# Kernel optimization log

Hardware: AMD Instinct MI355X
Metric: run time of the kernel (lower is better)

The kernel has to match this reference:

```python
import jax, jax.numpy as jnp
import numpy as np

N = 50000      # nodes
D = 128        # in_dim
O = 128        # out_dim
MAX_DEG = 32   # degrees uniform in [0, MAX_DEG]


def setup_inputs() -> dict:
    rng = np.random.default_rng(0)
    deg = rng.integers(0, MAX_DEG + 1, size=N)          # includes deg==0 nodes
    dst = np.repeat(np.arange(N), deg)                  # target node per edge (grouped, like the buckets)
    E = dst.shape[0]                                    # ~800000
    src = rng.integers(0, N, size=E)                    # neighbor index per edge (flat neighbor_list)

    key = jax.random.key(0)
    k1, k2, k3, k4 = jax.random.split(key, 4)
    scale = jnp.float32(1.0 / np.sqrt(D))
    return {
        "x":  jax.random.normal(k1, (N, D), jnp.float32),
        "Wg": jax.random.normal(k2, (O, D), jnp.float32) * scale,  # global_lin.weight
        "Wl": jax.random.normal(k3, (O, D), jnp.float32) * scale,  # local_lin.weight
        "Ws": jax.random.normal(k4, (O, D), jnp.float32) * scale,  # self_lin.weight
        "b":  jnp.zeros((O,), jnp.float32),                        # bias param
        "src": jnp.asarray(src, jnp.int32),
        "dst": jnp.asarray(dst, jnp.int32),
        "deg": jnp.asarray(deg, jnp.int32),
    }


def reference(x, Wg, Wl, Ws, b, src, dst, deg):
    n = x.shape[0]
    # global branch: applied to every node
    g_out = x @ Wg.T                                           # [N, O]
    # mean-aggregate neighbor features (gather + segment-sum == the per-bucket view().mean())
    neigh_sum = jax.ops.segment_sum(x[src], dst, num_segments=n)   # [N, D]
    degf = jnp.maximum(deg, 1).astype(x.dtype)[:, None]
    neigh_mean = neigh_sum * (1.0 / degf)                       # [N, D]
    # local + self branches only for deg > 0 (deg==0 bucket keeps just global_out)
    mask = (deg > 0).astype(x.dtype)[:, None]                   # [N, 1]
    out = g_out + mask * (neigh_mean @ Wl.T + x @ Ws.T) + b
    # dropout is identity in eval mode; ELU activation
    return jax.nn.elu(out)
```

## Files before the change

kernel.cpp:

```cpp
#include <hip/hip_runtime.h>
#include <cstdint>
#include <cstddef>

#define KCAT  384
#define AST   392
#define NPB   16
#define PREPV 128

typedef __attribute__((ext_vector_type(8))) short bf16x8;
typedef __attribute__((ext_vector_type(4))) float f32x4;

static __device__ __forceinline__ unsigned short f2bf(float f) {
    unsigned int u = __builtin_bit_cast(unsigned int, f);
    unsigned int lsb = (u >> 16) & 1u;
    u += 0x7fffu + lsb;
    return (unsigned short)(u >> 16);
}
static __device__ __forceinline__ float bfhi(unsigned int u) {
    return __builtin_bit_cast(float, u & 0xFFFF0000u);
}
static __device__ __forceinline__ float bflo(unsigned int u) {
    return __builtin_bit_cast(float, u << 16);
}
static __device__ __forceinline__ void acc8(float* a, const uint4& v) {
    a[0] += bflo(v.x); a[1] += bfhi(v.x); a[2] += bflo(v.y); a[3] += bfhi(v.y);
    a[4] += bflo(v.z); a[5] += bfhi(v.z); a[6] += bflo(v.w); a[7] += bfhi(v.w);
}

__global__ __launch_bounds__(256)
void prep(const float* __restrict__ x, const float* __restrict__ Wg,
          const float* __restrict__ Wl, const float* __restrict__ Ws,
          const int* __restrict__ dst, unsigned short* __restrict__ V,
          unsigned short* __restrict__ xb, int* __restrict__ blkoff,
          int total8, int nblk, int noffb, int E) {
    const int bx = blockIdx.x;
    const int t  = threadIdx.x;
    if (bx < PREPV) {
        const int o = bx;
        float v = (t < 128) ? Wg[o * 128 + t] : Wl[o * 128 + (t - 128)];
        V[o * KCAT + t] = f2bf(v);
        if (t < 128) V[o * KCAT + 256 + t] = f2bf(Ws[o * 128 + t]);
    } else if (bx < PREPV + noffb) {
        int b = (bx - PREPV) * 256 + t;
        if (b < nblk) {
            int target = b * NPB;
            int lo = 0, hi = E;
            while (lo < hi) { int mid = (lo + hi) >> 1; if (dst[mid] < target) lo = mid + 1; else hi = mid; }
            blkoff[b] = lo;
        }
    } else {
        int gid = (bx - PREPV - noffb) * 256 + t;
        if (gid < total8) {
            const float4* px = (const float4*)x + (size_t)gid * 2;
            float4 a = px[0], bq = px[1];
            uint4 u;
            u.x = (unsigned)f2bf(a.x)  | ((unsigned)f2bf(a.y)  << 16);
            u.y = (unsigned)f2bf(a.z)  | ((unsigned)f2bf(a.w)  << 16);
            u.z = (unsigned)f2bf(bq.x) | ((unsigned)f2bf(bq.y) << 16);
            u.w = (unsigned)f2bf(bq.z) | ((unsigned)f2bf(bq.w) << 16);
            ((uint4*)xb)[gid] = u;
        }
    }
}

__global__ __launch_bounds__(256, 8)
void fused_agg_gemm(const unsigned short* __restrict__ xb, const int* __restrict__ src,
                    const int* __restrict__ deg, const int* __restrict__ blkoff,
                    const unsigned short* __restrict__ V, const float* __restrict__ bias,
                    float* __restrict__ out, int N) {
    __shared__ __align__(16) unsigned short Ash[NPB * AST];
    __shared__ int sstart[NPB];
    __shared__ int sdeg[NPB];
    const int t    = threadIdx.x;
    const int wv   = t >> 6;
    const int lane = t & 63;
    const int c    = lane & 15;
    const int p    = lane >> 4;
    const int base = blockIdx.x * NPB;

    if (wv == 0) {
        int lo = blkoff[blockIdx.x];
        int n  = base + lane;
        int dg = (lane < NPB && n < N) ? deg[n] : 0;
        int incl = dg;
#pragma unroll
        for (int off = 1; off < NPB; off <<= 1) {
            int v = __shfl_up(incl, off, 64);
            if (lane >= off) incl += v;
        }
        if (lane < NPB) { sstart[lane] = lo + incl - dg; sdeg[lane] = dg; }
    }
    __syncthreads();

    const uint4* x4 = (const uint4*)xb;
    int dgs[4], sss[4], idxs[4];
#pragma unroll
    for (int r = 0; r < 4; ++r) {
        int row = wv * 4 + r;
        dgs[r] = sdeg[row];
        sss[r] = sstart[row];
        idxs[r] = 0;
        if (lane < dgs[r]) idxs[r] = src[sss[r] + lane];
    }
#pragma unroll
    for (int r = 0; r < 4; ++r) {
        const int row = wv * 4 + r;
        const int n   = base + row;
        const int d   = dgs[r];
        uint4 xv = {0, 0, 0, 0};
        if (p == 1 && n < N) xv = x4[(size_t)n * 16 + c];

        float a[8] = {0,0,0,0,0,0,0,0};
        float b[8] = {0,0,0,0,0,0,0,0};
        {
            int r0 = __shfl(idxs[r], p, 64);
            int r1 = __shfl(idxs[r], p + 4, 64);
            int r2 = __shfl(idxs[r], p + 8, 64);
            int r3 = __shfl(idxs[r], p + 12, 64);
            uint4 v0 = x4[(size_t)r0 * 16 + c];
            uint4 v1 = x4[(size_t)r1 * 16 + c];
            uint4 v2 = x4[(size_t)r2 * 16 + c];
            uint4 v3 = x4[(size_t)r3 * 16 + c];
            if (p < d)      acc8(a, v0);
            if (p + 4 < d)  acc8(b, v1);
            if (p + 8 < d)  acc8(a, v2);
            if (p + 12 < d) acc8(b, v3);
        }
        if (d > 16) {
            int e0 = 16 + p;
            int r0 = __shfl(idxs[r], e0, 64);
            int r1 = __shfl(idxs[r], e0 + 4, 64);
            int r2 = __shfl(idxs[r], e0 + 8, 64);
            int r3 = __shfl(idxs[r], e0 + 12, 64);
            uint4 v0 = x4[(size_t)r0 * 16 + c];
            uint4 v1 = x4[(size_t)r1 * 16 + c];
            uint4 v2 = x4[(size_t)r2 * 16 + c];
            uint4 v3 = x4[(size_t)r3 * 16 + c];
            if (e0 < d)      acc8(a, v0);
            if (e0 + 4 < d)  acc8(b, v1);
            if (e0 + 8 < d)  acc8(a, v2);
            if (e0 + 12 < d) acc8(b, v3);
        }
#pragma unroll
        for (int i = 0; i < 8; ++i) a[i] += b[i];
#pragma unroll
        for (int i = 0; i < 8; ++i) {
            a[i] += __shfl_xor(a[i], 16, 64);
            a[i] += __shfl_xor(a[i], 32, 64);
        }
        unsigned short* arow = Ash + row * AST;
        if (p == 0) {
            float inv = (d > 0) ? 1.0f / (float)d : 0.0f;
            uint4 u;
            u.x = (unsigned)f2bf(a[0]*inv) | ((unsigned)f2bf(a[1]*inv) << 16);
            u.y = (unsigned)f2bf(a[2]*inv) | ((unsigned)f2bf(a[3]*inv) << 16);
            u.z = (unsigned)f2bf(a[4]*inv) | ((unsigned)f2bf(a[5]*inv) << 16);
            u.w = (unsigned)f2bf(a[6]*inv) | ((unsigned)f2bf(a[7]*inv) << 16);
            *(uint4*)(arow + 128 + c * 8) = u;
        } else if (p == 1) {
            *(uint4*)(arow + c * 8) = xv;
            uint4 z = xv;
            if (d == 0) { z.x = 0; z.y = 0; z.z = 0; z.w = 0; }
            *(uint4*)(arow + 256 + c * 8) = z;
        }
    }
    __syncthreads();

    const int quad = lane >> 4;
    const int wcol = wv * 32;
    const unsigned short* V0 = V + (size_t)(wcol + c) * KCAT + quad * 8;
    const unsigned short* V1 = V + (size_t)(wcol + 16 + c) * KCAT + quad * 8;

    f32x4 acc0 = (f32x4){0.f, 0.f, 0.f, 0.f};
    f32x4 acc1 = (f32x4){0.f, 0.f, 0.f, 0.f};
    bf16x8 b0 = *(const bf16x8*)V0;
    bf16x8 b1 = *(const bf16x8*)V1;
    for (int k0 = 0; k0 < KCAT; k0 += 32) {
        int kn = (k0 + 32 < KCAT) ? k0 + 32 : 0;
        bf16x8 n0 = *(const bf16x8*)(V0 + kn);
        bf16x8 n1 = *(const bf16x8*)(V1 + kn);
        bf16x8 a0 = *(const bf16x8*)(Ash + (size_t)c * AST + k0 + quad * 8);
        acc0 = __builtin_amdgcn_mfma_f32_16x16x32_bf16(a0, b0, acc0, 0, 0, 0);
        acc1 = __builtin_amdgcn_mfma_f32_16x16x32_bf16(a0, b1, acc1, 0, 0, 0);
        b0 = n0; b1 = n1;
    }

    const int col0 = wcol + c, col1 = wcol + 16 + c;
    const float bv0 = bias[col0], bv1 = bias[col1];
#pragma unroll
    for (int reg = 0; reg < 4; ++reg) {
        int grow = base + quad * 4 + reg;
        if (grow < N) {
            float v0 = acc0[reg] + bv0;
            float v1 = acc1[reg] + bv1;
            out[(size_t)grow * 128 + col0] = (v0 > 0.f) ? v0 : expm1f(v0);
            out[(size_t)grow * 128 + col1] = (v1 > 0.f) ? v1 : expm1f(v1);
        }
    }
}

extern "C" void kernel_launch(void* const* d_in, const int* in_sizes, int n_in,
                              void* d_out, int out_size, void* d_ws, size_t ws_size,
                              hipStream_t stream) {
    const float* x  = (const float*)d_in[0];
    const float* Wg = (const float*)d_in[1];
    const float* Wl = (const float*)d_in[2];
    const float* Ws = (const float*)d_in[3];
    const float* b  = (const float*)d_in[4];
    const int*   src = (const int*)d_in[5];
    const int*   dst = (const int*)d_in[6];
    const int*   deg = (const int*)d_in[7];
    const int E = in_sizes[5];
    const int N = in_sizes[7];
    float* out = (float*)d_out;

    unsigned short* V      = (unsigned short*)d_ws;
    int*            blkoff = (int*)((char*)d_ws + 98304);
    unsigned short* xb     = (unsigned short*)((char*)d_ws + 98304 + 16384);

    const int nblk   = (N + NPB - 1) / NPB;
    const int noffb  = (nblk + 255) / 256;
    const int total8 = N * 16;
    const int nconv  = (total8 + 255) / 256;

    prep<<<dim3(PREPV + noffb + nconv), dim3(256), 0, stream>>>(
        x, Wg, Wl, Ws, dst, V, xb, blkoff, total8, nblk, noffb, E);
    fused_agg_gemm<<<dim3(nblk), dim3(256), 0, stream>>>(
        xb, src, deg, blkoff, V, b, out, N);
}
```

Before: 168.7 us.

## Split fused aggregate+GEMM into separate gather and GEMM kernels with pre-swizzled weights

```diff
diff --git a/kernel.cpp b/kernel.cpp
--- a/kernel.cpp
+++ b/kernel.cpp
@@ -2,54 +2,63 @@
 #include <cstdint>
 #include <cstddef>
 
-#define KCAT  384
-#define AST   392
-#define NPB   16
-#define PREPV 128
+#define KCAT 384
+#define GNPB 8
+#define MNPB 16
+#define GAST 264
+#define VP_BLOCKS 24
 
 typedef __attribute__((ext_vector_type(8))) short bf16x8;
 typedef __attribute__((ext_vector_type(4))) float f32x4;
 
 static __device__ __forceinline__ unsigned short f2bf(float f) {
     unsigned int u = __builtin_bit_cast(unsigned int, f);
-    unsigned int lsb = (u >> 16) & 1u;
-    u += 0x7fffu + lsb;
+    u += 0x7fffu + ((u >> 16) & 1u);
     return (unsigned short)(u >> 16);
 }
-static __device__ __forceinline__ float bfhi(unsigned int u) {
-    return __builtin_bit_cast(float, u & 0xFFFF0000u);
-}
-static __device__ __forceinline__ float bflo(unsigned int u) {
-    return __builtin_bit_cast(float, u << 16);
-}
-static __device__ __forceinline__ void acc8(float* a, const uint4& v) {
-    a[0] += bflo(v.x); a[1] += bfhi(v.x); a[2] += bflo(v.y); a[3] += bfhi(v.y);
-    a[4] += bflo(v.z); a[5] += bfhi(v.z); a[6] += bflo(v.w); a[7] += bfhi(v.w);
+static __device__ __forceinline__ float bfhi(unsigned int u) { return __builtin_bit_cast(float, u & 0xFFFF0000u); }
+static __device__ __forceinline__ float bflo(unsigned int u) { return __builtin_bit_cast(float, u << 16); }
+static __device__ __forceinline__ void acc8(float* a, const uint4& v, unsigned m) {
+    unsigned x0 = v.x & m, x1 = v.y & m, x2 = v.z & m, x3 = v.w & m;
+    a[0] += bflo(x0); a[1] += bfhi(x0); a[2] += bflo(x1); a[3] += bfhi(x1);
+    a[4] += bflo(x2); a[5] += bfhi(x2); a[6] += bflo(x3); a[7] += bfhi(x3);
 }
 
 __global__ __launch_bounds__(256)
 void prep(const float* __restrict__ x, const float* __restrict__ Wg,
           const float* __restrict__ Wl, const float* __restrict__ Ws,
-          const int* __restrict__ dst, unsigned short* __restrict__ V,
+          const int* __restrict__ dst, unsigned short* __restrict__ Vp,
           unsigned short* __restrict__ xb, int* __restrict__ blkoff,
-          int total8, int nblk, int noffb, int E) {
-    const int bx = blockIdx.x;
-    const int t  = threadIdx.x;
-    if (bx < PREPV) {
-        const int o = bx;
-        float v = (t < 128) ? Wg[o * 128 + t] : Wl[o * 128 + (t - 128)];
-        V[o * KCAT + t] = f2bf(v);
-        if (t < 128) V[o * KCAT + 256 + t] = f2bf(Ws[o * 128 + t]);
-    } else if (bx < PREPV + noffb) {
-        int b = (bx - PREPV) * 256 + t;
-        if (b < nblk) {
-            int target = b * NPB;
+          int total8, int nblk_g, int noffb, int E) {
+    const int bx = blockIdx.x, t = threadIdx.x;
+    if (bx < VP_BLOCKS) {
+        int gid = bx * 256 + t;
+        if (gid < 6144) {
+            int l = gid & 63, srow = (gid >> 6) % 12, g = gid / 768;
+            int o = g * 16 + (l & 15);
+            int k = srow * 32 + (l >> 4) * 8;
+            const float* w; int kk;
+            if (k < 128)      { w = Wg; kk = k; }
+            else if (k < 256) { w = Wl; kk = k - 128; }
+            else              { w = Ws; kk = k - 256; }
+            const float* p = w + o * 128 + kk;
+            uint4 u;
+            u.x = (unsigned)f2bf(p[0]) | ((unsigned)f2bf(p[1]) << 16);
+            u.y = (unsigned)f2bf(p[2]) | ((unsigned)f2bf(p[3]) << 16);
+            u.z = (unsigned)f2bf(p[4]) | ((unsigned)f2bf(p[5]) << 16);
+            u.w = (unsigned)f2bf(p[6]) | ((unsigned)f2bf(p[7]) << 16);
+            ((uint4*)Vp)[gid] = u;
+        }
+    } else if (bx < VP_BLOCKS + noffb) {
+        int b = (bx - VP_BLOCKS) * 256 + t;
+        if (b < nblk_g) {
+            int target = b * GNPB;
             int lo = 0, hi = E;
             while (lo < hi) { int mid = (lo + hi) >> 1; if (dst[mid] < target) lo = mid + 1; else hi = mid; }
             blkoff[b] = lo;
         }
     } else {
-        int gid = (bx - PREPV - noffb) * 256 + t;
+        int gid = (bx - VP_BLOCKS - noffb) * 256 + t;
         if (gid < total8) {
             const float4* px = (const float4*)x + (size_t)gid * 2;
             float4 a = px[0], bq = px[1];
@@ -63,129 +72,125 @@
     }
 }
 
-__global__ __launch_bounds__(256, 8)
-void fused_agg_gemm(const unsigned short* __restrict__ xb, const int* __restrict__ src,
-                    const int* __restrict__ deg, const int* __restrict__ blkoff,
-                    const unsigned short* __restrict__ V, const float* __restrict__ bias,
-                    float* __restrict__ out, int N) {
-    __shared__ __align__(16) unsigned short Ash[NPB * AST];
-    __shared__ int sstart[NPB];
-    __shared__ int sdeg[NPB];
-    const int t    = threadIdx.x;
-    const int wv   = t >> 6;
-    const int lane = t & 63;
-    const int c    = lane & 15;
-    const int p    = lane >> 4;
-    const int base = blockIdx.x * NPB;
-
-    if (wv == 0) {
-        int lo = blkoff[blockIdx.x];
-        int n  = base + lane;
-        int dg = (lane < NPB && n < N) ? deg[n] : 0;
-        int incl = dg;
-#pragma unroll
-        for (int off = 1; off < NPB; off <<= 1) {
-            int v = __shfl_up(incl, off, 64);
-            if (lane >= off) incl += v;
-        }
-        if (lane < NPB) { sstart[lane] = lo + incl - dg; sdeg[lane] = dg; }
+__global__ __launch_bounds__(512, 7)
+void gather(const unsigned short* __restrict__ xb, const int* __restrict__ src,
+            const int* __restrict__ deg, const int* __restrict__ blkoff,
+            unsigned short* __restrict__ M, int N) {
+    const int t = threadIdx.x, wv = t >> 6, lane = t & 63;
+    const int c = lane & 15, p = lane >> 4;
+    const int base = blockIdx.x * GNPB;
+
+    int dg8 = 0;
+    if (lane < GNPB && base + lane < N) dg8 = deg[base + lane];
+    int incl = dg8;
+#pragma unroll
+    for (int off = 1; off < GNPB; off <<= 1) {
+        int v = __shfl_up(incl, off, 64);
+        if (lane >= off) incl += v;
+    }
+    const int d = __shfl(dg8, wv, 64);
+    const int s = blkoff[blockIdx.x] + __shfl(incl, wv, 64) - d;
+    const int n = base + wv;
+    if (n >= N) return;
+
+    int idx = 0;
+    if (lane < d) idx = src[s + lane];
+
+    const uint4* x4 = (const uint4*)xb;
+    int r0 = __shfl(idx, p, 64),      r1 = __shfl(idx, p + 4, 64);
+    int r2 = __shfl(idx, p + 8, 64),  r3 = __shfl(idx, p + 12, 64);
+    uint4 v0 = x4[(size_t)r0 * 16 + c], v1 = x4[(size_t)r1 * 16 + c];
+    uint4 v2 = x4[(size_t)r2 * 16 + c], v3 = x4[(size_t)r3 * 16 + c];
+    uint4 v4, v5, v6, v7;
+    const bool two = (d > 16);
+    if (two) {
+        int e = 16 + p;
+        int r4 = __shfl(idx, e, 64),      r5 = __shfl(idx, e + 4, 64);
+        int r6 = __shfl(idx, e + 8, 64),  r7 = __shfl(idx, e + 12, 64);
+        v4 = x4[(size_t)r4 * 16 + c]; v5 = x4[(size_t)r5 * 16 + c];
+        v6 = x4[(size_t)r6 * 16 + c]; v7 = x4[(size_t)r7 * 16 + c];
+    }
+    float a[8] = {0,0,0,0,0,0,0,0};
+    float b[8] = {0,0,0,0,0,0,0,0};
+    acc8(a, v0, (p      < d) ? ~0u : 0u);
+    acc8(b, v1, (p + 4  < d) ? ~0u : 0u);
+    acc8(a, v2, (p + 8  < d) ? ~0u : 0u);
+    acc8(b, v3, (p + 12 < d) ? ~0u : 0u);
+    if (two) {
+        int e = 16 + p;
+        acc8(a, v4, (e      < d) ? ~0u : 0u);
+        acc8(b, v5, (e + 4  < d) ? ~0u : 0u);
+        acc8(a, v6, (e + 8  < d) ? ~0u : 0u);
+        acc8(b, v7, (e + 12 < d) ? ~0u : 0u);
+    }
+#pragma unroll
+    for (int i = 0; i < 8; ++i) a[i] += b[i];
+#pragma unroll
+    for (int i = 0; i < 8; ++i) {
+        a[i] += __shfl_xor(a[i], 16, 64);
+        a[i] += __shfl_xor(a[i], 32, 64);
+    }
+    if (p == 0) {
+        float inv = (d > 0) ? 1.0f / (float)d : 0.0f;
+        uint4 u;
+        u.x = (unsigned)f2bf(a[0]*inv) | ((unsigned)f2bf(a[1]*inv) << 16);
+        u.y = (unsigned)f2bf(a[2]*inv) | ((unsigned)f2bf(a[3]*inv) << 16);
+        u.z = (unsigned)f2bf(a[4]*inv) | ((unsigned)f2bf(a[5]*inv) << 16);
+        u.w = (unsigned)f2bf(a[6]*inv) | ((unsigned)f2bf(a[7]*inv) << 16);
+        ((uint4*)M)[(size_t)n * 16 + c] = u;
+    }
+}
+
+__global__ __launch_bounds__(256)
+void gemm(const unsigned short* __restrict__ xb, const unsigned short* __restrict__ Mm,
+          const int* __restrict__ deg, const unsigned short* __restrict__ Vp,
+          const float* __restrict__ bias, float* __restrict__ out, int N) {
+    __shared__ __align__(16) unsigned short As[MNPB * GAST];
+    __shared__ unsigned smask[MNPB];
+    const int t = threadIdx.x, wv = t >> 6, lane = t & 63;
+    const int c = lane & 15, quad = lane >> 4;
+    const int base = blockIdx.x * MNPB;
+
+    if (t < MNPB) smask[t] = (base + t < N && deg[base + t] > 0) ? 0xFFFFFFFFu : 0u;
+#pragma unroll
+    for (int it = 0; it < 2; ++it) {
+        int f = it * 256 + t;
+        int row = f >> 5, ch = f & 31;
+        int grow = base + row; if (grow > N - 1) grow = N - 1;
+        const unsigned short* gp = (ch < 16)
+            ? xb + (size_t)grow * 128 + ch * 8
+            : Mm + (size_t)grow * 128 + (ch - 16) * 8;
+        uint4 val = *(const uint4*)gp;
+        *(uint4*)(As + row * GAST + ch * 8) = val;
     }
     __syncthreads();
 
-    const uint4* x4 = (const uint4*)xb;
-    int dgs[4], sss[4], idxs[4];
-#pragma unroll
-    for (int r = 0; r < 4; ++r) {
-        int row = wv * 4 + r;
-        dgs[r] = sdeg[row];
-        sss[r] = sstart[row];
-        idxs[r] = 0;
-        if (lane < dgs[r]) idxs[r] = src[sss[r] + lane];
-    }
-#pragma unroll
-    for (int r = 0; r < 4; ++r) {
-        const int row = wv * 4 + r;
-        const int n   = base + row;
-        const int d   = dgs[r];
-        uint4 xv = {0, 0, 0, 0};
-        if (p == 1 && n < N) xv = x4[(size_t)n * 16 + c];
-
-        float a[8] = {0,0,0,0,0,0,0,0};
-        float b[8] = {0,0,0,0,0,0,0,0};
-        {
-            int r0 = __shfl(idxs[r], p, 64);
-            int r1 = __shfl(idxs[r], p + 4, 64);
-            int r2 = __shfl(idxs[r], p + 8, 64);
-            int r3 = __shfl(idxs[r], p + 12, 64);
-            uint4 v0 = x4[(size_t)r0 * 16 + c];
-            uint4 v1 = x4[(size_t)r1 * 16 + c];
-            uint4 v2 = x4[(size_t)r2 * 16 + c];
-            uint4 v3 = x4[(size_t)r3 * 16 + c];
-            if (p < d)      acc8(a, v0);
-            if (p + 4 < d)  acc8(b, v1);
-            if (p + 8 < d)  acc8(a, v2);
-            if (p + 12 < d) acc8(b, v3);
-        }
-        if (d > 16) {
-            int e0 = 16 + p;
-            int r0 = __shfl(idxs[r], e0, 64);
-            int r1 = __shfl(idxs[r], e0 + 4, 64);
-            int r2 = __shfl(idxs[r], e0 + 8, 64);
-            int r3 = __shfl(idxs[r], e0 + 12, 64);
-            uint4 v0 = x4[(size_t)r0 * 16 + c];
-            uint4 v1 = x4[(size_t)r1 * 16 + c];
-            uint4 v2 = x4[(size_t)r2 * 16 + c];
-            uint4 v3 = x4[(size_t)r3 * 16 + c];
-            if (e0 < d)      acc8(a, v0);
-            if (e0 + 4 < d)  acc8(b, v1);
-            if (e0 + 8 < d)  acc8(a, v2);
-            if (e0 + 12 < d) acc8(b, v3);
-        }
-#pragma unroll
-        for (int i = 0; i < 8; ++i) a[i] += b[i];
-#pragma unroll
-        for (int i = 0; i < 8; ++i) {
-            a[i] += __shfl_xor(a[i], 16, 64);
-            a[i] += __shfl_xor(a[i], 32, 64);
-        }
-        unsigned short* arow = Ash + row * AST;
-        if (p == 0) {
-            float inv = (d > 0) ? 1.0f / (float)d : 0.0f;
-            uint4 u;
-            u.x = (unsigned)f2bf(a[0]*inv) | ((unsigned)f2bf(a[1]*inv) << 16);
-            u.y = (unsigned)f2bf(a[2]*inv) | ((unsigned)f2bf(a[3]*inv) << 16);
-            u.z = (unsigned)f2bf(a[4]*inv) | ((unsigned)f2bf(a[5]*inv) << 16);
-            u.w = (unsigned)f2bf(a[6]*inv) | ((unsigned)f2bf(a[7]*inv) << 16);
-            *(uint4*)(arow + 128 + c * 8) = u;
-        } else if (p == 1) {
-            *(uint4*)(arow + c * 8) = xv;
-            uint4 z = xv;
-            if (d == 0) { z.x = 0; z.y = 0; z.z = 0; z.w = 0; }
-            *(uint4*)(arow + 256 + c * 8) = z;
-        }
-    }
-    __syncthreads();
-
-    const int quad = lane >> 4;
-    const int wcol = wv * 32;
-    const unsigned short* V0 = V + (size_t)(wcol + c) * KCAT + quad * 8;
-    const unsigned short* V1 = V + (size_t)(wcol + 16 + c) * KCAT + quad * 8;
+    const unsigned msk = smask[c];
+    const int g0 = 2 * wv, g1 = 2 * wv + 1;
+    const bf16x8* VB = (const bf16x8*)Vp;
 
     f32x4 acc0 = (f32x4){0.f, 0.f, 0.f, 0.f};
     f32x4 acc1 = (f32x4){0.f, 0.f, 0.f, 0.f};
-    bf16x8 b0 = *(const bf16x8*)V0;
-    bf16x8 b1 = *(const bf16x8*)V1;
-    for (int k0 = 0; k0 < KCAT; k0 += 32) {
-        int kn = (k0 + 32 < KCAT) ? k0 + 32 : 0;
-        bf16x8 n0 = *(const bf16x8*)(V0 + kn);
-        bf16x8 n1 = *(const bf16x8*)(V1 + kn);
-        bf16x8 a0 = *(const bf16x8*)(Ash + (size_t)c * AST + k0 + quad * 8);
+    bf16x8 b0 = VB[(g0 * 12) * 64 + lane];
+    bf16x8 b1 = VB[(g1 * 12) * 64 + lane];
+#pragma unroll
+    for (int s2 = 0; s2 < 12; ++s2) {
+        int sn = (s2 + 1 < 12) ? s2 + 1 : 0;
+        bf16x8 n0 = VB[(g0 * 12 + sn) * 64 + lane];
+        bf16x8 n1 = VB[(g1 * 12 + sn) * 64 + lane];
+        int seg = s2 >> 2, kk = (s2 & 3) * 32;
+        bf16x8 a0 = *(const bf16x8*)(As + c * GAST + (seg == 1 ? 128 : 0) + kk + quad * 8);
+        if (seg == 2) {
+            uint4 ai = __builtin_bit_cast(uint4, a0);
+            ai.x &= msk; ai.y &= msk; ai.z &= msk; ai.w &= msk;
+            a0 = __builtin_bit_cast(bf16x8, ai);
+        }
         acc0 = __builtin_amdgcn_mfma_f32_16x16x32_bf16(a0, b0, acc0, 0, 0, 0);
         acc1 = __builtin_amdgcn_mfma_f32_16x16x32_bf16(a0, b1, acc1, 0, 0, 0);
         b0 = n0; b1 = n1;
     }
 
-    const int col0 = wcol + c, col1 = wcol + 16 + c;
+    const int col0 = g0 * 16 + c, col1 = g1 * 16 + c;
     const float bv0 = bias[col0], bv1 = bias[col1];
 #pragma unroll
     for (int reg = 0; reg < 4; ++reg) {
@@ -193,8 +198,8 @@
         if (grow < N) {
             float v0 = acc0[reg] + bv0;
             float v1 = acc1[reg] + bv1;
-            out[(size_t)grow * 128 + col0] = (v0 > 0.f) ? v0 : expm1f(v0);
-            out[(size_t)grow * 128 + col1] = (v1 > 0.f) ? v1 : expm1f(v1);
+            out[(size_t)grow * 128 + col0] = (v0 > 0.f) ? v0 : __expf(v0) - 1.0f;
+            out[(size_t)grow * 128 + col1] = (v1 > 0.f) ? v1 : __expf(v1) - 1.0f;
         }
     }
 }
@@ -214,17 +219,19 @@
     const int N = in_sizes[7];
     float* out = (float*)d_out;
 
-    unsigned short* V      = (unsigned short*)d_ws;
+    const size_t NB = (size_t)N * 128 * 2;
+    unsigned short* Vp     = (unsigned short*)d_ws;
     int*            blkoff = (int*)((char*)d_ws + 98304);
-    unsigned short* xb     = (unsigned short*)((char*)d_ws + 98304 + 16384);
-
-    const int nblk   = (N + NPB - 1) / NPB;
-    const int noffb  = (nblk + 255) / 256;
+    unsigned short* xb     = (unsigned short*)((char*)d_ws + 131072);
+    unsigned short* Mm     = (unsigned short*)((char*)d_ws + 131072 + NB);
+
+    const int nblk_g = (N + GNPB - 1) / GNPB;
+    const int noffb  = (nblk_g + 255) / 256;
     const int total8 = N * 16;
     const int nconv  = (total8 + 255) / 256;
 
-    prep<<<dim3(PREPV + noffb + nconv), dim3(256), 0, stream>>>(
-        x, Wg, Wl, Ws, dst, V, xb, blkoff, total8, nblk, noffb, E);
-    fused_agg_gemm<<<dim3(nblk), dim3(256), 0, stream>>>(
-        xb, src, deg, blkoff, V, b, out, N);
-}
+    prep<<<dim3(VP_BLOCKS + noffb + nconv), dim3(256), 0, stream>>>(
+        x, Wg, Wl, Ws, dst, Vp, xb, blkoff, total8, nblk_g, noffb, E);
+    gather<<<dim3(nblk_g), dim3(512), 0, stream>>>(xb, src, deg, blkoff, Mm, N);
+    gemm<<<dim3((N + MNPB - 1) / MNPB), dim3(256), 0, stream>>>(xb, Mm, deg, Vp, b, out, N);
+}
```

Measured after the change: 141.4 us. 1.19x faster.
